# Kernel optimization log

Measured on AMD Instinct MI355X. Metric: run time of the kernel, lower is better.

Reference implementation:

```python
import jax, jax.numpy as jnp
import numpy as np

N_NODES = 50000
N_EDGES = 800000
IN_C = 64
OUT_C = 64
HEADS = 4
N_LAYERS = 2
BN_EPS = 1e-5
NEG_SLOPE = 0.2


def setup_inputs() -> dict:
    key = jax.random.key(0)
    ks = jax.random.split(key, 20)
    inp = {
        "x": jax.random.normal(ks[0], (N_NODES, IN_C), dtype=jnp.float32),
        "edge_index": jax.random.randint(ks[1], (2, N_EDGES), 0, N_NODES, dtype=jnp.int64),
        "edge_weight": jax.random.uniform(ks[2], (N_EDGES,), dtype=jnp.float32),
    }
    # per-layer GATConv + BN params (glorot-ish init)
    for i in range(N_LAYERS):
        k = 3 + i * 5
        scale = 1.0 / np.sqrt(IN_C)
        inp[f"W{i}"] = jax.random.normal(ks[k], (IN_C, HEADS * OUT_C), dtype=jnp.float32) * scale
        inp[f"asrc{i}"] = jax.random.normal(ks[k + 1], (HEADS, OUT_C), dtype=jnp.float32) * scale
        inp[f"adst{i}"] = jax.random.normal(ks[k + 2], (HEADS, OUT_C), dtype=jnp.float32) * scale
        inp[f"b{i}"] = jnp.zeros((OUT_C,), dtype=jnp.float32)
        inp[f"gamma{i}"] = jnp.ones((OUT_C,), dtype=jnp.float32)
        inp[f"beta{i}"] = jnp.zeros((OUT_C,), dtype=jnp.float32)
    return inp


def _gat_layer(x, src, dst, W, a_src, a_dst, b):
    # x: [N, C_in]; src/dst: [E'] (with self loops). Per-head dim = OUT_C.
    xh = (x @ W).reshape(-1, HEADS, OUT_C)          # [N, H, C]
    al_src = jnp.sum(xh * a_src[None], axis=-1)      # [N, H]
    al_dst = jnp.sum(xh * a_dst[None], axis=-1)      # [N, H]
    e = jax.nn.leaky_relu(al_src[src] + al_dst[dst], NEG_SLOPE)  # [E', H]
    # segment softmax over edges sharing a destination node
    m = jax.lax.stop_gradient(jax.ops.segment_max(e, dst, num_segments=N_NODES))
    p = jnp.exp(e - m[dst])
    denom = jax.ops.segment_sum(p, dst, num_segments=N_NODES)
    alpha = p / (denom[dst] + 1e-16)                 # [E', H]
    out = jax.ops.segment_sum(alpha[:, :, None] * xh[src], dst, num_segments=N_NODES)  # [N,H,C]
    return out.mean(axis=1) + b                      # concat=False -> mean over heads


def _batchnorm(x, gamma, beta):
    mu = x.mean(axis=0)
    var = x.var(axis=0)
    return gamma * (x - mu) * jax.lax.rsqrt(var + BN_EPS) + beta


def reference(x, edge_index, edge_weight, W0, asrc0, adst0, b0, gamma0, beta0,
              W1, asrc1, adst1, b1, gamma1, beta1):
    # edge_weight is passed as edge_attr to PyG GATConv but edge_dim=None -> ignored.
    loop = jnp.arange(N_NODES, dtype=edge_index.dtype)
    src = jnp.concatenate([edge_index[0], loop])  # add_self_loops=True (PyG default)
    dst = jnp.concatenate([edge_index[1], loop])
    params = [(W0, asrc0, adst0, b0, gamma0, beta0),
              (W1, asrc1, adst1, b1, gamma1, beta1)]
    saved = None
    for (W, a_s, a_d, b, g, bt) in params:
        x = _gat_layer(x, src, dst, W, a_s, a_d, b)
        saved = x
        x = _batchnorm(x, g, bt)
        x = jax.nn.relu(x)
        # dropout(0.5) is identity in eval mode
    return (x, saved)
```

## Files before the change

### kernel.cpp

```cpp
#include <hip/hip_runtime.h>
#include <stdint.h>

#define NEG_SLOPE 0.2f
#define BN_EPS 1e-5f

typedef __attribute__((ext_vector_type(8))) short bf16x8;
typedef __attribute__((ext_vector_type(4))) float f32x4;

__device__ __forceinline__ float bf2f(unsigned short u) {
  union { unsigned int i; float f; } v; v.i = ((unsigned int)u) << 16; return v.f;
}
__device__ __forceinline__ float asf(unsigned int u) {
  union { unsigned int i; float f; } v; v.i = u; return v.f;
}
__device__ __forceinline__ unsigned short f2bf(float f) {
  union { float f; unsigned int i; } v; v.f = f;
  unsigned int i = v.i;
  return (unsigned short)((i + 0x7fffu + ((i >> 16) & 1u)) >> 16);
}
__device__ __forceinline__ float loadF(const void* p, long long i, int f32) {
  return f32 ? ((const float*)p)[i] : bf2f(((const unsigned short*)p)[i]);
}
__device__ __forceinline__ int edge_at(const void* ei, long long idx, int is64) {
  return is64 ? (int)((const long long*)ei)[idx] : ((const int*)ei)[idx];
}

__global__ void detect_kernel(const unsigned short* __restrict__ x,
                              const int* __restrict__ ei32,
                              int* __restrict__ flags) {
  __shared__ int wild, oddnz;
  if (threadIdx.x == 0) { wild = 0; oddnz = 0; }
  __syncthreads();
  int lw = 0, lo = 0;
  for (int i = threadIdx.x; i < 4096; i += 256) {
    unsigned short u = x[i];
    int ex = (u >> 7) & 0xFF;
    if (ex >= 0x86) lw++;
    if (ei32[2 * i + 1] != 0) lo++;
  }
  if (lw) atomicAdd(&wild, lw);
  if (lo) atomicAdd(&oddnz, lo);
  __syncthreads();
  if (threadIdx.x == 0) { flags[0] = (wild > 64) ? 1 : 0; flags[1] = (oddnz == 0) ? 1 : 0; }
}

__global__ __launch_bounds__(256) void wtrans_kernel(
    const void* __restrict__ W0, const void* __restrict__ as0, const void* __restrict__ ad0,
    const void* __restrict__ W1, const void* __restrict__ as1, const void* __restrict__ ad1,
    const int* __restrict__ flags,
    unsigned short* __restrict__ WTx0, unsigned short* __restrict__ WTx1) {
  const void* W = blockIdx.x ? W1 : W0;
  const void* asrc = blockIdx.x ? as1 : as0;
  const void* adst = blockIdx.x ? ad1 : ad0;
  unsigned short* WTx = blockIdx.x ? WTx1 : WTx0;
  int f32 = flags[0];
  __shared__ unsigned short Wl[64 * 258];
  int t = threadIdx.x;
  for (int i = t; i < 64 * 256; i += 256) {
    int k = i >> 8, c = i & 255;
    Wl[k * 258 + c] = f32 ? f2bf(((const float*)W)[i]) : ((const unsigned short*)W)[i];
  }
  __syncthreads();
  {
    int c = t;
    #pragma unroll
    for (int k8 = 0; k8 < 64; k8 += 8) {
      unsigned int p0 = (unsigned int)Wl[(k8 + 0) * 258 + c] | ((unsigned int)Wl[(k8 + 1) * 258 + c] << 16);
      unsigned int p1 = (unsigned int)Wl[(k8 + 2) * 258 + c] | ((unsigned int)Wl[(k8 + 3) * 258 + c] << 16);
      unsigned int p2 = (unsigned int)Wl[(k8 + 4) * 258 + c] | ((unsigned int)Wl[(k8 + 5) * 258 + c] << 16);
      unsigned int p3 = (unsigned int)Wl[(k8 + 6) * 258 + c] | ((unsigned int)Wl[(k8 + 7) * 258 + c] << 16);
      uint4 pk; pk.x = p0; pk.y = p1; pk.z = p2; pk.w = p3;
      *(uint4*)&WTx[c * 64 + k8] = pk;
    }
  }
  for (int idx = t; idx < 512; idx += 256) {
    int r = idx >> 6;
    int k = idx & 63;
    int h = r & 3;
    const void* av = (r >> 2) ? adst : asrc;
    float acc = 0.f;
    #pragma unroll 8
    for (int c = 0; c < 64; c++)
      acc += bf2f(Wl[k * 258 + h * 64 + c]) * loadF(av, h * 64 + c, f32);
    WTx[(256 + r) * 64 + k] = f2bf(acc);
  }
  for (int idx = t; idx < 512; idx += 256) WTx[264 * 64 + idx] = 0;
}

__global__ __launch_bounds__(256) void hist_kernel(const void* __restrict__ ei, int E, int N,
                                                   const int* __restrict__ flags,
                                                   int* __restrict__ deg) {
  int e = blockIdx.x * 256 + threadIdx.x;
  if (e >= E) return;
  int is64 = flags[1];
  int d = edge_at(ei, (long long)E + e, is64);
  d = (d < 0 || d >= N) ? 0 : d;
  atomicAdd(&deg[d], 1);
}

__global__ __launch_bounds__(256) void partial_kernel(const int* __restrict__ deg,
                                                      int* __restrict__ blocksum, int N) {
  int t = threadIdx.x;
  int idx = blockIdx.x * 256 + t;
  int v = (idx < N) ? deg[idx] : 0;
  #pragma unroll
  for (int o = 1; o < 64; o <<= 1) v += __shfl_xor(v, o);
  __shared__ int ws[4];
  if ((t & 63) == 0) ws[t >> 6] = v;
  __syncthreads();
  if (t == 0) blocksum[blockIdx.x] = ws[0] + ws[1] + ws[2] + ws[3];
}

__global__ void scan_base_kernel(const int* __restrict__ blocksum,
                                 int* __restrict__ blockbase, int B) {
  int lane = threadIdx.x;
  int base = 0;
  if (lane == 0) blockbase[0] = 0;
  for (int start = 0; start < B; start += 64) {
    int idx = start + lane;
    int v = (idx < B) ? blocksum[idx] : 0;
    int sc = v;
    #pragma unroll
    for (int o = 1; o < 64; o <<= 1) {
      int u = __shfl_up(sc, o);
      if (lane >= o) sc += u;
    }
    if (idx < B) blockbase[idx + 1] = base + sc;
    base = __shfl(base + sc, 63);
  }
}

__global__ __launch_bounds__(256) void scan_final_kernel(const int* __restrict__ deg,
                                                         const int* __restrict__ blockbase,
                                                         int* __restrict__ offsets, int N) {
  int t = threadIdx.x;
  int lane = t & 63;
  int wid = t >> 6;
  int idx = blockIdx.x * 256 + t;
  int v = (idx < N) ? deg[idx] : 0;
  int sc = v;
  #pragma unroll
  for (int o = 1; o < 64; o <<= 1) {
    int u = __shfl_up(sc, o);
    if (lane >= o) sc += u;
  }
  __shared__ int ws[4];
  if (lane == 63) ws[wid] = sc;
  __syncthreads();
  int add = 0;
  #pragma unroll
  for (int w = 0; w < 4; w++) if (w < wid) add += ws[w];
  if (idx < N) offsets[idx + 1] = blockbase[blockIdx.x] + add + sc;
  if (idx == 0) offsets[0] = 0;
}

__global__ __launch_bounds__(256) void scatter_kernel(
    const void* __restrict__ ei, int E, int N, const int* __restrict__ flags,
    const int* __restrict__ offsets, int* __restrict__ cursor,
    int* __restrict__ csr_src) {
  int e = blockIdx.x * 256 + threadIdx.x;
  if (e >= E) return;
  int is64 = flags[1];
  int s = edge_at(ei, e, is64);
  int d = edge_at(ei, (long long)E + e, is64);
  s = (s < 0 || s >= N) ? 0 : s;
  d = (d < 0 || d >= N) ? 0 : d;
  int pos = offsets[d] + atomicAdd(&cursor[d], 1);
  csr_src[pos] = s;
}

__global__ __launch_bounds__(256, 2) void gemm_mfma(
    const void* __restrict__ x, const unsigned short* __restrict__ WTx,
    const int* __restrict__ flags, int mode,
    const float* __restrict__ gsum, const float* __restrict__ gsq,
    const void* __restrict__ gamma, const void* __restrict__ beta,
    unsigned short* __restrict__ xh, float* __restrict__ als, float* __restrict__ ald,
    int N) {
  __shared__ unsigned short RP[4][16 * 264];
  __shared__ float bnsc[64], bnsh[64];
  int f32 = flags[0];
  int t = threadIdx.x;
  if (mode == 1) {
    if (t < 64) {
      float mu = gsum[t] / (float)N;
      float var = fmaxf(gsq[t] / (float)N - mu * mu, 0.f);
      float sc = loadF(gamma, t, f32) * rsqrtf(var + BN_EPS);
      bnsc[t] = sc;
      bnsh[t] = loadF(beta, t, f32) - mu * sc;
    }
    __syncthreads();
  }
  int wave = t >> 6, lane = t & 63;
  int q = lane >> 4, r16 = lane & 15;
  int m0 = blockIdx.x * 64 + wave * 16;
  if (m0 >= N) return;
  int row = m0 + r16;
  int rowc = row < N ? row : N - 1;

  bf16x8 a0, a1;
  if (mode == 1) {
    const float* xp = (const float*)x + (size_t)rowc * 64 + q * 8;
    float va[8], vb[8];
    *(float4*)&va[0] = ((const float4*)xp)[0];
    *(float4*)&va[4] = ((const float4*)xp)[1];
    *(float4*)&vb[0] = ((const float4*)(xp + 32))[0];
    *(float4*)&vb[4] = ((const float4*)(xp + 32))[1];
    int k0 = q * 8;
    #pragma unroll
    for (int jj = 0; jj < 8; jj++) {
      float v = fmaxf(va[jj] * bnsc[k0 + jj] + bnsh[k0 + jj], 0.f);
      float w = fmaxf(vb[jj] * bnsc[k0 + 32 + jj] + bnsh[k0 + 32 + jj], 0.f);
      a0[jj] = (short)f2bf(v);
      a1[jj] = (short)f2bf(w);
    }
  } else if (f32) {
    const float* xp = (const float*)x + (size_t)rowc * 64 + q * 8;
    float va[8], vb[8];
    *(float4*)&va[0] = ((const float4*)xp)[0];
    *(float4*)&va[4] = ((const float4*)xp)[1];
    *(float4*)&vb[0] = ((const float4*)(xp + 32))[0];
    *(float4*)&vb[4] = ((const float4*)(xp + 32))[1];
    #pragma unroll
    for (int jj = 0; jj < 8; jj++) {
      a0[jj] = (short)f2bf(va[jj]);
      a1[jj] = (short)f2bf(vb[jj]);
    }
  } else {
    const unsigned short* xp = (const unsigned short*)x + (size_t)rowc * 64 + q * 8;
    a0 = *(const bf16x8*)xp;
    a1 = *(const bf16x8*)(xp + 32);
  }

  f32x4 acc[17];
  #pragma unroll
  for (int tt = 0; tt < 17; tt++) acc[tt] = (f32x4){0.f, 0.f, 0.f, 0.f};
  #pragma unroll
  for (int tt = 0; tt < 17; tt++) {
    int c = tt * 16 + r16;
    bf16x8 b0 = *(const bf16x8*)(WTx + c * 64 + q * 8);
    bf16x8 b1 = *(const bf16x8*)(WTx + c * 64 + 32 + q * 8);
    acc[tt] = __builtin_amdgcn_mfma_f32_16x16x32_bf16(a0, b0, acc[tt], 0, 0, 0);
    acc[tt] = __builtin_amdgcn_mfma_f32_16x16x32_bf16(a1, b1, acc[tt], 0, 0, 0);
  }

  {
    int obase = m0 + q * 4;
    #pragma unroll
    for (int rr = 0; rr < 4; rr++) {
      int orow = obase + rr;
      if (orow < N) {
        if (r16 < 4) als[orow * 4 + r16] = acc[16][rr];
        else if (r16 < 8) ald[orow * 4 + (r16 - 4)] = acc[16][rr];
      }
    }
  }
  unsigned short* rp = RP[wave];
  #pragma unroll
  for (int tt = 0; tt < 16; tt++) {
    #pragma unroll
    for (int rr = 0; rr < 4; rr++)
      rp[(q * 4 + rr) * 264 + tt * 16 + r16] = f2bf(acc[tt][rr]);
  }
  #pragma unroll
  for (int i = 0; i < 8; i++) {
    int g = i * 64 + lane;
    int r = g >> 5;
    int grp = g & 31;
    uint4 v = *(const uint4*)&rp[r * 264 + grp * 8];
    int orow = m0 + r;
    if (orow < N) ((uint4*)xh)[(size_t)orow * 32 + grp] = v;
  }
}

__global__ __launch_bounds__(256) void agg_kernel(
    const unsigned short* __restrict__ xh,
    const float* __restrict__ als, const float* __restrict__ ald,
    const int* __restrict__ offsets, const int* __restrict__ csr_src,
    const void* __restrict__ bias, const int* __restrict__ flags,
    float* __restrict__ y, float* __restrict__ gsum, float* __restrict__ gsq, int N) {
  __shared__ float bsum[64], bsq[64];
  int t = threadIdx.x;
  if (t < 64) { bsum[t] = 0.f; bsq[t] = 0.f; }
  __syncthreads();
  int lane = t & 63;
  int wid = t >> 6;
  int h = lane >> 4;
  int f32 = flags[0];
  const uint2* xv = (const uint2*)xh;
  float rs0 = 0.f, rs1 = 0.f, rs2 = 0.f, rs3 = 0.f;
  float rq0 = 0.f, rq1 = 0.f, rq2 = 0.f, rq3 = 0.f;
  int stride = gridDim.x * 4;
  for (int n = blockIdx.x * 4 + wid; n < N; n += stride) {
    float ad = ald[n * 4 + h];
    float e = als[n * 4 + h] + ad;
    e = (e > 0.f) ? e : NEG_SLOPE * e;
    float p = __expf(e);
    float dsum = p;
    uint2 xs = xv[(size_t)n * 64 + lane];
    float a0 = p * asf(xs.x << 16), a1 = p * asf(xs.x & 0xffff0000u);
    float a2 = p * asf(xs.y << 16), a3 = p * asf(xs.y & 0xffff0000u);
    int beg = offsets[n], end = offsets[n + 1];
    int j = beg;
    for (; j + 4 <= end; j += 4) {
      int s0 = csr_src[j];
      int s1 = csr_src[j + 1];
      int s2 = csr_src[j + 2];
      int s3 = csr_src[j + 3];
      uint2 v0 = xv[(size_t)s0 * 64 + lane];
      uint2 v1 = xv[(size_t)s1 * 64 + lane];
      uint2 v2 = xv[(size_t)s2 * 64 + lane];
      uint2 v3 = xv[(size_t)s3 * 64 + lane];
      float e0 = als[s0 * 4 + h] + ad;
      float e1 = als[s1 * 4 + h] + ad;
      float e2 = als[s2 * 4 + h] + ad;
      float e3 = als[s3 * 4 + h] + ad;
      e0 = (e0 > 0.f) ? e0 : NEG_SLOPE * e0;
      e1 = (e1 > 0.f) ? e1 : NEG_SLOPE * e1;
      e2 = (e2 > 0.f) ? e2 : NEG_SLOPE * e2;
      e3 = (e3 > 0.f) ? e3 : NEG_SLOPE * e3;
      float p0 = __expf(e0);
      float p1 = __expf(e1);
      float p2 = __expf(e2);
      float p3 = __expf(e3);
      dsum += p0 + p1 + p2 + p3;
      a0 += p0 * asf(v0.x << 16) + p1 * asf(v1.x << 16)
          + p2 * asf(v2.x << 16) + p3 * asf(v3.x << 16);
      a1 += p0 * asf(v0.x & 0xffff0000u) + p1 * asf(v1.x & 0xffff0000u)
          + p2 * asf(v2.x & 0xffff0000u) + p3 * asf(v3.x & 0xffff0000u);
      a2 += p0 * asf(v0.y << 16) + p1 * asf(v1.y << 16)
          + p2 * asf(v2.y << 16) + p3 * asf(v3.y << 16);
      a3 += p0 * asf(v0.y & 0xffff0000u) + p1 * asf(v1.y & 0xffff0000u)
          + p2 * asf(v2.y & 0xffff0000u) + p3 * asf(v3.y & 0xffff0000u);
    }
    for (; j < end; j++) {
      int s0 = csr_src[j];
      uint2 v0 = xv[(size_t)s0 * 64 + lane];
      float e0 = als[s0 * 4 + h] + ad;
      e0 = (e0 > 0.f) ? e0 : NEG_SLOPE * e0;
      float p0 = __expf(e0);
      dsum += p0;
      a0 += p0 * asf(v0.x << 16);
      a1 += p0 * asf(v0.x & 0xffff0000u);
      a2 += p0 * asf(v0.y << 16);
      a3 += p0 * asf(v0.y & 0xffff0000u);
    }
    float inv = 1.0f / dsum;
    a0 *= inv; a1 *= inv; a2 *= inv; a3 *= inv;
    a0 += __shfl_xor(a0, 16); a0 += __shfl_xor(a0, 32);
    a1 += __shfl_xor(a1, 16); a1 += __shfl_xor(a1, 32);
    a2 += __shfl_xor(a2, 16); a2 += __shfl_xor(a2, 32);
    a3 += __shfl_xor(a3, 16); a3 += __shfl_xor(a3, 32);
    if (lane < 16) {
      float4 o;
      o.x = 0.25f * a0 + loadF(bias, 4 * lane + 0, f32);
      o.y = 0.25f * a1 + loadF(bias, 4 * lane + 1, f32);
      o.z = 0.25f * a2 + loadF(bias, 4 * lane + 2, f32);
      o.w = 0.25f * a3 + loadF(bias, 4 * lane + 3, f32);
      ((float4*)(y + (size_t)n * 64))[lane] = o;
      rs0 += o.x; rs1 += o.y; rs2 += o.z; rs3 += o.w;
      rq0 += o.x * o.x; rq1 += o.y * o.y; rq2 += o.z * o.z; rq3 += o.w * o.w;
    }
  }
  if (lane < 16) {
    atomicAdd(&bsum[4 * lane + 0], rs0);
    atomicAdd(&bsum[4 * lane + 1], rs1);
    atomicAdd(&bsum[4 * lane + 2], rs2);
    atomicAdd(&bsum[4 * lane + 3], rs3);
    atomicAdd(&bsq[4 * lane + 0], rq0);
    atomicAdd(&bsq[4 * lane + 1], rq1);
    atomicAdd(&bsq[4 * lane + 2], rq2);
    atomicAdd(&bsq[4 * lane + 3], rq3);
  }
  __syncthreads();
  if (t < 64) {
    atomicAdd(&gsum[t], bsum[t]);
    atomicAdd(&gsq[t], bsq[t]);
  }
}

__global__ __launch_bounds__(256) void bn_kernel(
    const float* __restrict__ y, const float* __restrict__ gsum, const float* __restrict__ gsq,
    const void* __restrict__ gamma, const void* __restrict__ beta,
    const int* __restrict__ flags, float* __restrict__ out_f, int N) {
  int i = blockIdx.x * 256 + threadIdx.x;
  if (i >= N * 16) return;
  int f32 = flags[0];
  int cg = i & 15;
  float4 v = ((const float4*)y)[i];
  float4 s = ((const float4*)gsum)[cg];
  float4 q = ((const float4*)gsq)[cg];
  float inv_n = 1.0f / (float)N;
  float vv[4] = {v.x, v.y, v.z, v.w};
  float ss[4] = {s.x, s.y, s.z, s.w};
  float qq[4] = {q.x, q.y, q.z, q.w};
  float o[4];
  #pragma unroll
  for (int k = 0; k < 4; k++) {
    float g = loadF(gamma, 4 * cg + k, f32);
    float b = loadF(beta, 4 * cg + k, f32);
    float mu = ss[k] * inv_n;
    float var = fmaxf(qq[k] * inv_n - mu * mu, 0.f);
    float r = g * (vv[k] - mu) * rsqrtf(var + BN_EPS) + b;
    o[k] = r > 0.f ? r : 0.f;
  }
  float4 ov; ov.x = o[0]; ov.y = o[1]; ov.z = o[2]; ov.w = o[3];
  ((float4*)out_f)[i] = ov;
}

extern "C" void kernel_launch(void* const* d_in, const int* in_sizes, int n_in,
                              void* d_out, int out_size, void* d_ws, size_t ws_size,
                              hipStream_t stream) {
  const void* x    = d_in[0];
  const void* ei   = d_in[1];
  const void* W0    = d_in[3];
  const void* asrc0 = d_in[4];
  const void* adst0 = d_in[5];
  const void* b0    = d_in[6];
  const void* g0    = d_in[7];
  const void* be0   = d_in[8];
  const void* W1    = d_in[9];
  const void* asrc1 = d_in[10];
  const void* adst1 = d_in[11];
  const void* b1    = d_in[12];
  const void* g1    = d_in[13];
  const void* be1   = d_in[14];

  int N = in_sizes[0] / 64;
  int E = in_sizes[1] / 2;
  int NB = (N + 255) / 256;
  int NG = (N + 63) / 64;
  int NA = (N + 15) / 16;

  char* p = (char*)d_ws;
  auto alloc = [&](size_t bytes) -> char* {
    char* r = p;
    p += (bytes + 255) & ~(size_t)255;
    return r;
  };
  int* flags    = (int*)alloc(256);
  int* deg      = (int*)alloc((size_t)N * 4);
  int* cursor   = (int*)alloc((size_t)N * 4);
  int* offsets  = (int*)alloc((size_t)(N + 1) * 4);
  int* blocksum = (int*)alloc((size_t)NB * 4);
  int* blockbase= (int*)alloc((size_t)(NB + 1) * 4);
  int* csr_src  = (int*)alloc((size_t)E * 4);
  unsigned short* WTx0 = (unsigned short*)alloc(272 * 64 * 2);
  unsigned short* WTx1 = (unsigned short*)alloc(272 * 64 * 2);
  unsigned short* xh = (unsigned short*)alloc((size_t)N * 256 * 2);
  float* als    = (float*)alloc((size_t)N * 4 * 4);
  float* ald    = (float*)alloc((size_t)N * 4 * 4);
  float* y      = (float*)alloc((size_t)N * 64 * 4);
  float* gsum0  = (float*)alloc(256);
  float* gsq0   = (float*)alloc(256);
  float* gsum1  = (float*)alloc(256);
  float* gsq1   = (float*)alloc(256);

  hipMemsetAsync(deg, 0, (size_t)N * 4, stream);
  hipMemsetAsync(cursor, 0, (size_t)N * 4, stream);
  hipMemsetAsync(gsum0, 0, 1024, stream);

  detect_kernel<<<1, 256, 0, stream>>>((const unsigned short*)x, (const int*)ei, flags);
  wtrans_kernel<<<2, 256, 0, stream>>>(W0, asrc0, adst0, W1, asrc1, adst1, flags, WTx0, WTx1);

  hist_kernel<<<(E + 255) / 256, 256, 0, stream>>>(ei, E, N, flags, deg);
  partial_kernel<<<NB, 256, 0, stream>>>(deg, blocksum, N);
  scan_base_kernel<<<1, 64, 0, stream>>>(blocksum, blockbase, NB);
  scan_final_kernel<<<NB, 256, 0, stream>>>(deg, blockbase, offsets, N);
  scatter_kernel<<<(E + 255) / 256, 256, 0, stream>>>(ei, E, N, flags, offsets, cursor, csr_src);

  float* out_x = (float*)d_out;
  float* out_saved = out_x + (size_t)N * 64;

  gemm_mfma<<<NG, 256, 0, stream>>>(x, WTx0, flags, 0, (const float*)nullptr,
                                    (const float*)nullptr, nullptr, nullptr,
                                    xh, als, ald, N);
  agg_kernel<<<NA, 256, 0, stream>>>(xh, als, ald, offsets, csr_src, b0, flags,
                                     y, gsum0, gsq0, N);
  gemm_mfma<<<NG, 256, 0, stream>>>(y, WTx1, flags, 1, gsum0, gsq0, g0, be0,
                                    xh, als, ald, N);
  agg_kernel<<<NA, 256, 0, stream>>>(xh, als, ald, offsets, csr_src, b1, flags,
                                     out_saved, gsum1, gsq1, N);
  bn_kernel<<<(N * 16 + 255) / 256, 256, 0, stream>>>(out_saved, gsum1, gsq1, g1, be1,
                                                      flags, out_x, N);
}
```

Before: 518.8 us.

## Split BN stats from aggregation, one node per wave, shrink GEMM LDS staging

The aggregation kernel now handles one destination node per wave with no grid-stride loop or in-kernel BN statistic reduction, and its edge unroll drops from 4 to 2. A separate stats_kernel re-reads the output to compute per-channel sums and squared sums. The GEMM epilogue stages output through a smaller LDS buffer in four column chunks and raises the occupancy hint to 3 blocks per CU. The aim is higher occupancy and less register and LDS pressure, at the cost of an extra pass over y and fewer loads in flight per wave.

```diff
diff --git a/kernel.cpp b/kernel.cpp
--- a/kernel.cpp
+++ b/kernel.cpp
@@ -169,14 +169,14 @@
   csr_src[pos] = s;
 }
 
-__global__ __launch_bounds__(256, 2) void gemm_mfma(
+__global__ __launch_bounds__(256, 3) void gemm_mfma(
     const void* __restrict__ x, const unsigned short* __restrict__ WTx,
     const int* __restrict__ flags, int mode,
     const float* __restrict__ gsum, const float* __restrict__ gsq,
     const void* __restrict__ gamma, const void* __restrict__ beta,
     unsigned short* __restrict__ xh, float* __restrict__ als, float* __restrict__ ald,
     int N) {
-  __shared__ unsigned short RP[4][16 * 264];
+  __shared__ unsigned short RP[4][16 * 68];
   __shared__ float bnsc[64], bnsh[64];
   int f32 = flags[0];
   int t = threadIdx.x;
@@ -256,19 +256,23 @@
   }
   unsigned short* rp = RP[wave];
   #pragma unroll
-  for (int tt = 0; tt < 16; tt++) {
-    #pragma unroll
-    for (int rr = 0; rr < 4; rr++)
-      rp[(q * 4 + rr) * 264 + tt * 16 + r16] = f2bf(acc[tt][rr]);
-  }
-  #pragma unroll
-  for (int i = 0; i < 8; i++) {
-    int g = i * 64 + lane;
-    int r = g >> 5;
-    int grp = g & 31;
-    uint4 v = *(const uint4*)&rp[r * 264 + grp * 8];
-    int orow = m0 + r;
-    if (orow < N) ((uint4*)xh)[(size_t)orow * 32 + grp] = v;
+  for (int g4 = 0; g4 < 4; g4++) {
+    #pragma unroll
+    for (int tt2 = 0; tt2 < 4; tt2++) {
+      int tile = g4 * 4 + tt2;
+      #pragma unroll
+      for (int rr = 0; rr < 4; rr++)
+        rp[(q * 4 + rr) * 68 + tt2 * 16 + r16] = f2bf(acc[tile][rr]);
+    }
+    #pragma unroll
+    for (int i = 0; i < 2; i++) {
+      int g = i * 64 + lane;
+      int r = g >> 3;
+      int grp = g & 7;
+      uint4 v = *(const uint4*)&rp[r * 68 + grp * 8];
+      int orow = m0 + r;
+      if (orow < N) ((uint4*)xh)[(size_t)orow * 32 + g4 * 8 + grp] = v;
+    }
   }
 }
 
@@ -277,104 +281,88 @@
     const float* __restrict__ als, const float* __restrict__ ald,
     const int* __restrict__ offsets, const int* __restrict__ csr_src,
     const void* __restrict__ bias, const int* __restrict__ flags,
-    float* __restrict__ y, float* __restrict__ gsum, float* __restrict__ gsq, int N) {
-  __shared__ float bsum[64], bsq[64];
+    float* __restrict__ y, int N) {
+  int lane = threadIdx.x & 63;
+  int wid = threadIdx.x >> 6;
+  int n = blockIdx.x * 4 + wid;
+  if (n >= N) return;
+  int h = lane >> 4;
+  const uint2* xv = (const uint2*)xh;
+  float ad = ald[n * 4 + h];
+  float e = als[n * 4 + h] + ad;
+  e = (e > 0.f) ? e : NEG_SLOPE * e;
+  float p = __expf(e);
+  float dsum = p;
+  uint2 xs = xv[(size_t)n * 64 + lane];
+  float a0 = p * asf(xs.x << 16), a1 = p * asf(xs.x & 0xffff0000u);
+  float a2 = p * asf(xs.y << 16), a3 = p * asf(xs.y & 0xffff0000u);
+  int beg = offsets[n], end = offsets[n + 1];
+  int j = beg;
+  for (; j + 2 <= end; j += 2) {
+    int s0 = csr_src[j];
+    int s1 = csr_src[j + 1];
+    uint2 v0 = xv[(size_t)s0 * 64 + lane];
+    uint2 v1 = xv[(size_t)s1 * 64 + lane];
+    float e0 = als[s0 * 4 + h] + ad;
+    float e1 = als[s1 * 4 + h] + ad;
+    e0 = (e0 > 0.f) ? e0 : NEG_SLOPE * e0;
+    e1 = (e1 > 0.f) ? e1 : NEG_SLOPE * e1;
+    float p0 = __expf(e0);
+    float p1 = __expf(e1);
+    dsum += p0 + p1;
+    a0 += p0 * asf(v0.x << 16) + p1 * asf(v1.x << 16);
+    a1 += p0 * asf(v0.x & 0xffff0000u) + p1 * asf(v1.x & 0xffff0000u);
+    a2 += p0 * asf(v0.y << 16) + p1 * asf(v1.y << 16);
+    a3 += p0 * asf(v0.y & 0xffff0000u) + p1 * asf(v1.y & 0xffff0000u);
+  }
+  if (j < end) {
+    int s0 = csr_src[j];
+    uint2 v0 = xv[(size_t)s0 * 64 + lane];
+    float e0 = als[s0 * 4 + h] + ad;
+    e0 = (e0 > 0.f) ? e0 : NEG_SLOPE * e0;
+    float p0 = __expf(e0);
+    dsum += p0;
+    a0 += p0 * asf(v0.x << 16);
+    a1 += p0 * asf(v0.x & 0xffff0000u);
+    a2 += p0 * asf(v0.y << 16);
+    a3 += p0 * asf(v0.y & 0xffff0000u);
+  }
+  float inv = 1.0f / dsum;
+  a0 *= inv; a1 *= inv; a2 *= inv; a3 *= inv;
+  a0 += __shfl_xor(a0, 16); a0 += __shfl_xor(a0, 32);
+  a1 += __shfl_xor(a1, 16); a1 += __shfl_xor(a1, 32);
+  a2 += __shfl_xor(a2, 16); a2 += __shfl_xor(a2, 32);
+  a3 += __shfl_xor(a3, 16); a3 += __shfl_xor(a3, 32);
+  if (lane < 16) {
+    int f32 = flags[0];
+    float4 o;
+    o.x = 0.25f * a0 + loadF(bias, 4 * lane + 0, f32);
+    o.y = 0.25f * a1 + loadF(bias, 4 * lane + 1, f32);
+    o.z = 0.25f * a2 + loadF(bias, 4 * lane + 2, f32);
+    o.w = 0.25f * a3 + loadF(bias, 4 * lane + 3, f32);
+    ((float4*)(y + (size_t)n * 64))[lane] = o;
+  }
+}
+
+__global__ __launch_bounds__(256) void stats_kernel(const float* __restrict__ y,
+                                                    float* __restrict__ gsum,
+                                                    float* __restrict__ gsq, int N) {
+  __shared__ float ls[256], lq[256];
   int t = threadIdx.x;
-  if (t < 64) { bsum[t] = 0.f; bsq[t] = 0.f; }
-  __syncthreads();
-  int lane = t & 63;
-  int wid = t >> 6;
-  int h = lane >> 4;
-  int f32 = flags[0];
-  const uint2* xv = (const uint2*)xh;
-  float rs0 = 0.f, rs1 = 0.f, rs2 = 0.f, rs3 = 0.f;
-  float rq0 = 0.f, rq1 = 0.f, rq2 = 0.f, rq3 = 0.f;
-  int stride = gridDim.x * 4;
-  for (int n = blockIdx.x * 4 + wid; n < N; n += stride) {
-    float ad = ald[n * 4 + h];
-    float e = als[n * 4 + h] + ad;
-    e = (e > 0.f) ? e : NEG_SLOPE * e;
-    float p = __expf(e);
-    float dsum = p;
-    uint2 xs = xv[(size_t)n * 64 + lane];
-    float a0 = p * asf(xs.x << 16), a1 = p * asf(xs.x & 0xffff0000u);
-    float a2 = p * asf(xs.y << 16), a3 = p * asf(xs.y & 0xffff0000u);
-    int beg = offsets[n], end = offsets[n + 1];
-    int j = beg;
-    for (; j + 4 <= end; j += 4) {
-      int s0 = csr_src[j];
-      int s1 = csr_src[j + 1];
-      int s2 = csr_src[j + 2];
-      int s3 = csr_src[j + 3];
-      uint2 v0 = xv[(size_t)s0 * 64 + lane];
-      uint2 v1 = xv[(size_t)s1 * 64 + lane];
-      uint2 v2 = xv[(size_t)s2 * 64 + lane];
-      uint2 v3 = xv[(size_t)s3 * 64 + lane];
-      float e0 = als[s0 * 4 + h] + ad;
-      float e1 = als[s1 * 4 + h] + ad;
-      float e2 = als[s2 * 4 + h] + ad;
-      float e3 = als[s3 * 4 + h] + ad;
-      e0 = (e0 > 0.f) ? e0 : NEG_SLOPE * e0;
-      e1 = (e1 > 0.f) ? e1 : NEG_SLOPE * e1;
-      e2 = (e2 > 0.f) ? e2 : NEG_SLOPE * e2;
-      e3 = (e3 > 0.f) ? e3 : NEG_SLOPE * e3;
-      float p0 = __expf(e0);
-      float p1 = __expf(e1);
-      float p2 = __expf(e2);
-      float p3 = __expf(e3);
-      dsum += p0 + p1 + p2 + p3;
-      a0 += p0 * asf(v0.x << 16) + p1 * asf(v1.x << 16)
-          + p2 * asf(v2.x << 16) + p3 * asf(v3.x << 16);
-      a1 += p0 * asf(v0.x & 0xffff0000u) + p1 * asf(v1.x & 0xffff0000u)
-          + p2 * asf(v2.x & 0xffff0000u) + p3 * asf(v3.x & 0xffff0000u);
-      a2 += p0 * asf(v0.y << 16) + p1 * asf(v1.y << 16)
-          + p2 * asf(v2.y << 16) + p3 * asf(v3.y << 16);
-      a3 += p0 * asf(v0.y & 0xffff0000u) + p1 * asf(v1.y & 0xffff0000u)
-          + p2 * asf(v2.y & 0xffff0000u) + p3 * asf(v3.y & 0xffff0000u);
-    }
-    for (; j < end; j++) {
-      int s0 = csr_src[j];
-      uint2 v0 = xv[(size_t)s0 * 64 + lane];
-      float e0 = als[s0 * 4 + h] + ad;
-      e0 = (e0 > 0.f) ? e0 : NEG_SLOPE * e0;
-      float p0 = __expf(e0);
-      dsum += p0;
-      a0 += p0 * asf(v0.x << 16);
-      a1 += p0 * asf(v0.x & 0xffff0000u);
-      a2 += p0 * asf(v0.y << 16);
-      a3 += p0 * asf(v0.y & 0xffff0000u);
-    }
-    float inv = 1.0f / dsum;
-    a0 *= inv; a1 *= inv; a2 *= inv; a3 *= inv;
-    a0 += __shfl_xor(a0, 16); a0 += __shfl_xor(a0, 32);
-    a1 += __shfl_xor(a1, 16); a1 += __shfl_xor(a1, 32);
-    a2 += __shfl_xor(a2, 16); a2 += __shfl_xor(a2, 32);
-    a3 += __shfl_xor(a3, 16); a3 += __shfl_xor(a3, 32);
-    if (lane < 16) {
-      float4 o;
-      o.x = 0.25f * a0 + loadF(bias, 4 * lane + 0, f32);
-      o.y = 0.25f * a1 + loadF(bias, 4 * lane + 1, f32);
-      o.z = 0.25f * a2 + loadF(bias, 4 * lane + 2, f32);
-      o.w = 0.25f * a3 + loadF(bias, 4 * lane + 3, f32);
-      ((float4*)(y + (size_t)n * 64))[lane] = o;
-      rs0 += o.x; rs1 += o.y; rs2 += o.z; rs3 += o.w;
-      rq0 += o.x * o.x; rq1 += o.y * o.y; rq2 += o.z * o.z; rq3 += o.w * o.w;
-    }
-  }
-  if (lane < 16) {
-    atomicAdd(&bsum[4 * lane + 0], rs0);
-    atomicAdd(&bsum[4 * lane + 1], rs1);
-    atomicAdd(&bsum[4 * lane + 2], rs2);
-    atomicAdd(&bsum[4 * lane + 3], rs3);
-    atomicAdd(&bsq[4 * lane + 0], rq0);
-    atomicAdd(&bsq[4 * lane + 1], rq1);
-    atomicAdd(&bsq[4 * lane + 2], rq2);
-    atomicAdd(&bsq[4 * lane + 3], rq3);
-  }
+  int c = t & 63;
+  int r0 = blockIdx.x * 4 + (t >> 6);
+  float s = 0.f, q = 0.f;
+  for (int r = r0; r < N; r += gridDim.x * 4) {
+    float v = y[(size_t)r * 64 + c];
+    s += v; q += v * v;
+  }
+  ls[t] = s; lq[t] = q;
   __syncthreads();
   if (t < 64) {
-    atomicAdd(&gsum[t], bsum[t]);
-    atomicAdd(&gsq[t], bsq[t]);
+    s = ls[t] + ls[t + 64] + ls[t + 128] + ls[t + 192];
+    q = lq[t] + lq[t + 64] + lq[t + 128] + lq[t + 192];
+    atomicAdd(&gsum[c], s);
+    atomicAdd(&gsq[c], q);
   }
 }
 
@@ -429,7 +417,7 @@
   int E = in_sizes[1] / 2;
   int NB = (N + 255) / 256;
   int NG = (N + 63) / 64;
-  int NA = (N + 15) / 16;
+  int NA = (N + 3) / 4;
 
   char* p = (char*)d_ws;
   auto alloc = [&](size_t bytes) -> char* {
@@ -474,12 +462,12 @@
   gemm_mfma<<<NG, 256, 0, stream>>>(x, WTx0, flags, 0, (const float*)nullptr,
                                     (const float*)nullptr, nullptr, nullptr,
                                     xh, als, ald, N);
-  agg_kernel<<<NA, 256, 0, stream>>>(xh, als, ald, offsets, csr_src, b0, flags,
-                                     y, gsum0, gsq0, N);
+  agg_kernel<<<NA, 256, 0, stream>>>(xh, als, ald, offsets, csr_src, b0, flags, y, N);
+  stats_kernel<<<250, 256, 0, stream>>>(y, gsum0, gsq0, N);
   gemm_mfma<<<NG, 256, 0, stream>>>(y, WTx1, flags, 1, gsum0, gsq0, g0, be0,
                                     xh, als, ald, N);
-  agg_kernel<<<NA, 256, 0, stream>>>(xh, als, ald, offsets, csr_src, b1, flags,
-                                     out_saved, gsum1, gsq1, N);
+  agg_kernel<<<NA, 256, 0, stream>>>(xh, als, ald, offsets, csr_src, b1, flags, out_saved, N);
+  stats_kernel<<<250, 256, 0, stream>>>(out_saved, gsum1, gsq1, N);
   bn_kernel<<<(N * 16 + 255) / 256, 256, 0, stream>>>(out_saved, gsum1, gsq1, g1, be1,
                                                       flags, out_x, N);
 }
```

After: 457.9 us. -11.7%, faster.
